# Kernel optimization log

Hardware: AMD Instinct MI355X
Metric: run time of the kernel (lower is better)

The kernel has to match this reference:

```python
import jax, jax.numpy as jnp
import numpy as np

N_NODES = 20000
N_EDGES = 320000
D_IN = 256
D_HID = 256
D_OUT = 128
N_LAYERS = 5
BN_EPS = 1e-5
W_SCALE = 1.0 / np.sqrt(D_HID)


def setup_inputs() -> dict:
    key = jax.random.key(0)
    ks = jax.random.split(key, 16)
    x = jax.random.normal(ks[0], (N_NODES, D_IN), dtype=jnp.float32)
    edge_index = jax.random.randint(ks[1], (2, N_EDGES), 0, N_NODES, dtype=jnp.int32)
    W1 = jax.random.normal(ks[2], (N_LAYERS, D_IN, D_HID), dtype=jnp.float32) * W_SCALE
    b1 = jax.random.normal(ks[3], (N_LAYERS, D_HID), dtype=jnp.float32) * 0.01
    W2a = jax.random.normal(ks[4], (N_LAYERS - 1, D_HID, D_HID), dtype=jnp.float32) * W_SCALE
    b2a = jax.random.normal(ks[5], (N_LAYERS - 1, D_HID), dtype=jnp.float32) * 0.01
    W2_last = jax.random.normal(ks[6], (D_HID, D_OUT), dtype=jnp.float32) * W_SCALE
    b2_last = jax.random.normal(ks[7], (D_OUT,), dtype=jnp.float32) * 0.01
    eps = jnp.zeros((N_LAYERS,), dtype=jnp.float32)
    bn_gamma = jnp.ones((N_LAYERS - 1, D_HID), dtype=jnp.float32)
    bn_beta = jnp.zeros((N_LAYERS - 1, D_HID), dtype=jnp.float32)
    bn_mean = jax.random.normal(ks[8], (N_LAYERS - 1, D_HID), dtype=jnp.float32) * 0.1
    bn_var = jax.random.uniform(ks[9], (N_LAYERS - 1, D_HID), dtype=jnp.float32, minval=0.5, maxval=1.5)
    return {"x": x, "edge_index": edge_index, "W1": W1, "b1": b1, "W2a": W2a,
            "b2a": b2a, "W2_last": W2_last, "b2_last": b2_last, "eps": eps,
            "bn_gamma": bn_gamma, "bn_beta": bn_beta, "bn_mean": bn_mean, "bn_var": bn_var}


def reference(x, edge_index, W1, b1, W2a, b2a, W2_last, b2_last, eps,
              bn_gamma, bn_beta, bn_mean, bn_var):
    src, dst = edge_index[0], edge_index[1]
    n = x.shape[0]

    def gin_conv(h, e, w1, bb1, w2, bb2):
        # scatter-add neighbor sum: agg[v] = sum_{(u->v)} h[u]
        agg = jax.ops.segment_sum(h[src], dst, num_segments=n)  # [N, d]
        z = (1.0 + e) * h + agg
        z = jax.nn.relu(z @ w1 + bb1)
        return z @ w2 + bb2

    h = x
    for i in range(N_LAYERS - 1):
        h = gin_conv(h, eps[i], W1[i], b1[i], W2a[i], b2a[i])
        # BatchNorm1d in eval mode (running stats); dropout inactive at inference
        h = (h - bn_mean[i]) * jax.lax.rsqrt(bn_var[i] + BN_EPS) * bn_gamma[i] + bn_beta[i]
        h = jax.nn.relu(h)
    out = gin_conv(h, eps[N_LAYERS - 1], W1[N_LAYERS - 1], b1[N_LAYERS - 1], W2_last, b2_last)
    return out
```

## Files before the change

kernel.cpp:

```cpp
#include <hip/hip_runtime.h>
#include <stdint.h>

#define NN    20000
#define NE    320000
#define MPAD  20096
#define DD    256
#define DOUT  128
#define CAP   64
#define RS    40
#define SS    1288
#define STS   264
#define SFS   132

typedef unsigned short u16;
typedef __attribute__((ext_vector_type(8))) __bf16 bf16x8;
typedef __attribute__((ext_vector_type(4))) float  f32x4;

__device__ __forceinline__ uint32_t f2b(float f){
  union { float f; uint32_t u; } x; x.f = f;
  uint32_t r = x.u + 0x7FFFu + ((x.u >> 16) & 1u);
  return r >> 16;
}
__device__ __forceinline__ float blo(uint32_t p){ union{uint32_t u;float f;}x; x.u=p<<16;         return x.f; }
__device__ __forceinline__ float bhi(uint32_t p){ union{uint32_t u;float f;}x; x.u=p&0xFFFF0000u; return x.f; }
__device__ __forceinline__ int   fiu(float f){ union{float f;int i;}x; x.f=f; return x.i; }
__device__ __forceinline__ float uif(int i){ union{int i;float f;}x; x.i=i; return x.f; }

#define TB 152
#define XB (MPAD/4)
#define EB ((NE+255)/256)
__global__ __launch_bounds__(256) void prep_all(
    const float* __restrict__ x, const int* __restrict__ src, const int* __restrict__ dst,
    const float* __restrict__ W1, const float* __restrict__ W2a, const float* __restrict__ W2l,
    u16* __restrict__ W1t, u16* __restrict__ W2at, u16* __restrict__ W2lt,
    u16* __restrict__ h0, int* __restrict__ cnt, int* __restrict__ csr)
{
  __shared__ u16 Ts[64][65];
  int b = blockIdx.x, tid = threadIdx.x;
  if (b < TB){
    const float* srcp; u16* dstp; int ldS, k0, n0;
    if (b < 80){
      int layer = b >> 4, sub = b & 15;
      srcp = W1 + layer*65536; dstp = W1t + layer*65536; ldS = 256;
      k0 = (sub >> 2)*64; n0 = (sub & 3)*64;
    } else if (b < 144){
      int bb = b - 80; int layer = bb >> 4, sub = bb & 15;
      srcp = W2a + layer*65536; dstp = W2at + layer*65536; ldS = 256;
      k0 = (sub >> 2)*64; n0 = (sub & 3)*64;
    } else {
      int sub = b - 144;
      srcp = W2l; dstp = W2lt; ldS = 128;
      k0 = (sub >> 1)*64; n0 = (sub & 1)*64;
    }
    int c = tid & 63, r0 = tid >> 6;
    #pragma unroll
    for (int i = 0; i < 16; ++i){
      int r = r0 + i*4;
      Ts[r][c] = (u16)f2b(srcp[(size_t)(k0 + r)*ldS + n0 + c]);
    }
    __syncthreads();
    #pragma unroll
    for (int i = 0; i < 16; ++i){
      int n = r0 + i*4;
      dstp[(size_t)(n0 + n)*256 + k0 + c] = Ts[c][n];
    }
  } else if (b < TB + XB){
    int bb = b - TB;
    int row  = bb*4 + (tid >> 6);
    int lane = tid & 63;
    uint2 o = make_uint2(0u, 0u);
    if (row < NN){
      float4 f = *(const float4*)(x + (size_t)row*DD + lane*4);
      o.x = f2b(f.x) | (f2b(f.y) << 16);
      o.y = f2b(f.z) | (f2b(f.w) << 16);
    }
    *(uint2*)(h0 + (size_t)row*DD + lane*4) = o;
  } else {
    int e = (b - TB - XB)*256 + tid;
    if (e < NE){
      int d = dst[e];
      int slot = atomicAdd(&cnt[d], 1);
      if (slot < CAP) csr[d*CAP + slot] = src[e];
    }
  }
}

__global__ __launch_bounds__(256, 3) void gin_fused(
    const u16* __restrict__ hin, const int* __restrict__ cnt, const int* __restrict__ csr,
    const float* __restrict__ eps_arr, int layer,
    const u16* __restrict__ w1, const float* __restrict__ b1,
    const u16* __restrict__ w2, const float* __restrict__ b2,
    const float* __restrict__ gma, const float* __restrict__ bta,
    const float* __restrict__ mu,  const float* __restrict__ var,
    u16* __restrict__ hout, float* __restrict__ outf, int last)
{
  __shared__ __align__(16) u16 As[8*SS];
  int tid  = threadIdx.x;
  int lane = tid & 63, w = tid >> 6;
  int m0 = blockIdx.x * 32;
  int l15 = lane & 15, l4 = lane >> 4;

  {
    float e = 1.0f + eps_arr[layer];
    int half = lane >> 5, kl = lane & 31;
    int xi = (lane ^ 32) << 2;
    const u16* hrow = hin + kl*8;
    u16* dstL = As + (kl >> 2)*SS + (kl & 3)*8;
    for (int i = 0; i < 8; ++i){
      int row = w*8 + i;
      int v = __builtin_amdgcn_readfirstlane(m0 + row);
      float a0=0.f,a1=0.f,a2=0.f,a3=0.f,a4=0.f,a5=0.f,a6=0.f,a7=0.f;
      if (v < NN){
        uint4 ov = *(const uint4*)(hrow + (size_t)v*DD);
        int deg = cnt[v]; deg = deg > CAP ? CAP : deg;
        const int* lst = csr + (size_t)v*CAP;
        for (int base = 0; base < deg; base += 16){
          int4 q[4];
          #pragma unroll
          for (int c = 0; c < 4; ++c) q[c] = *(const int4*)(lst + base + 4*c);
          int idv[8];
          #pragma unroll
          for (int c = 0; c < 4; ++c){
            idv[2*c]   = half ? q[c].y : q[c].x;
            idv[2*c+1] = half ? q[c].w : q[c].z;
          }
          uint4 rv[8];
          #pragma unroll
          for (int c = 0; c < 8; ++c){
            int g = (base + 2*c + half < deg) ? idv[c] : v;
            rv[c] = *(const uint4*)(hrow + (size_t)g*DD);
          }
          #pragma unroll
          for (int c = 0; c < 8; ++c){
            if (base + 2*c + half < deg){
              a0 += blo(rv[c].x); a1 += bhi(rv[c].x);
              a2 += blo(rv[c].y); a3 += bhi(rv[c].y);
              a4 += blo(rv[c].z); a5 += bhi(rv[c].z);
              a6 += blo(rv[c].w); a7 += bhi(rv[c].w);
            }
          }
        }
        float eh = half ? 0.0f : e;
        a0 += eh*blo(ov.x); a1 += eh*bhi(ov.x);
        a2 += eh*blo(ov.y); a3 += eh*bhi(ov.y);
        a4 += eh*blo(ov.z); a5 += eh*bhi(ov.z);
        a6 += eh*blo(ov.w); a7 += eh*bhi(ov.w);
      }
      a0 += uif(__builtin_amdgcn_ds_bpermute(xi, fiu(a0)));
      a1 += uif(__builtin_amdgcn_ds_bpermute(xi, fiu(a1)));
      a2 += uif(__builtin_amdgcn_ds_bpermute(xi, fiu(a2)));
      a3 += uif(__builtin_amdgcn_ds_bpermute(xi, fiu(a3)));
      a4 += uif(__builtin_amdgcn_ds_bpermute(xi, fiu(a4)));
      a5 += uif(__builtin_amdgcn_ds_bpermute(xi, fiu(a5)));
      a6 += uif(__builtin_amdgcn_ds_bpermute(xi, fiu(a6)));
      a7 += uif(__builtin_amdgcn_ds_bpermute(xi, fiu(a7)));
      if (half == 0){
        uint4 o;
        o.x = f2b(a0) | (f2b(a1) << 16);
        o.y = f2b(a2) | (f2b(a3) << 16);
        o.z = f2b(a4) | (f2b(a5) << 16);
        o.w = f2b(a6) | (f2b(a7) << 16);
        *(uint4*)(dstL + row*RS) = o;
      }
    }
  }
  __syncthreads();

  f32x4 acc1[4][2];
  #pragma unroll
  for (int i=0;i<4;++i)
    #pragma unroll
    for (int j=0;j<2;++j){ f32x4 zr={0.f,0.f,0.f,0.f}; acc1[i][j]=zr; }
  {
    int hidb = w*64;
    for (int s = 0; s < 8; ++s){
      bf16x8 af[4], bz[2];
      #pragma unroll
      for (int mi=0;mi<4;++mi)
        af[mi] = *(const bf16x8*)(w1 + (size_t)(hidb + mi*16 + l15)*DD + s*32 + l4*8);
      #pragma unroll
      for (int nj=0;nj<2;++nj)
        bz[nj] = *(const bf16x8*)(As + s*SS + (nj*16 + l15)*RS + l4*8);
      #pragma unroll
      for (int mi=0;mi<4;++mi)
        #pragma unroll
        for (int nj=0;nj<2;++nj)
          acc1[mi][nj] = __builtin_amdgcn_mfma_f32_16x16x32_bf16(af[mi], bz[nj], acc1[mi][nj], 0,0,0);
    }
  }
  __syncthreads();

  {
    int hidb = w*64;
    #pragma unroll
    for (int mi=0;mi<4;++mi){
      float4 bv = *(const float4*)(b1 + hidb + mi*16 + l4*4);
      int s2 = w*2 + (mi >> 1);
      int kp = (mi & 1)*16 + l4*4;
      #pragma unroll
      for (int nj=0;nj<2;++nj){
        int zrow = nj*16 + l15;
        float v0 = acc1[mi][nj][0] + bv.x; v0 = v0 > 0.f ? v0 : 0.f;
        float v1 = acc1[mi][nj][1] + bv.y; v1 = v1 > 0.f ? v1 : 0.f;
        float v2 = acc1[mi][nj][2] + bv.z; v2 = v2 > 0.f ? v2 : 0.f;
        float v3 = acc1[mi][nj][3] + bv.w; v3 = v3 > 0.f ? v3 : 0.f;
        uint2 pk;
        pk.x = f2b(v0) | (f2b(v1) << 16);
        pk.y = f2b(v2) | (f2b(v3) << 16);
        *(uint2*)(As + s2*SS + zrow*RS + kp) = pk;
      }
    }
  }
  __syncthreads();

  if (!last){
    f32x4 acc2[2][4];
    #pragma unroll
    for (int i=0;i<2;++i)
      #pragma unroll
      for (int j=0;j<4;++j){ f32x4 zr={0.f,0.f,0.f,0.f}; acc2[i][j]=zr; }
    int cb = w*64;
    for (int s = 0; s < 8; ++s){
      bf16x8 at[2], bw[4];
      #pragma unroll
      for (int i=0;i<2;++i)
        at[i] = *(const bf16x8*)(As + s*SS + (i*16 + l15)*RS + l4*8);
      #pragma unroll
      for (int j=0;j<4;++j)
        bw[j] = *(const bf16x8*)(w2 + (size_t)(cb + j*16 + l15)*DD + s*32 + l4*8);
      #pragma unroll
      for (int i=0;i<2;++i)
        #pragma unroll
        for (int j=0;j<4;++j)
          acc2[i][j] = __builtin_amdgcn_mfma_f32_16x16x32_bf16(at[i], bw[j], acc2[i][j], 0,0,0);
    }
    __syncthreads();
    u16* St = As;
    #pragma unroll
    for (int j=0;j<4;++j){
      int col = cb + j*16 + l15;
      float sc = rsqrtf(var[col] + 1e-5f) * gma[col];
      float sh = (b2[col] - mu[col]) * sc + bta[col];
      #pragma unroll
      for (int i=0;i<2;++i){
        #pragma unroll
        for (int r=0;r<4;++r){
          int row = i*16 + l4*4 + r;
          float vv = acc2[i][j][r]*sc + sh;
          vv = vv > 0.f ? vv : 0.f;
          St[row*STS + col] = (u16)f2b(vv);
        }
      }
    }
    __syncthreads();
    #pragma unroll
    for (int it = 0; it < 4; ++it){
      int idx = it*256 + tid;
      int row = idx >> 5, c = idx & 31;
      *(uint4*)(hout + (size_t)(m0 + row)*DD + c*8) = *(const uint4*)(St + row*STS + c*8);
    }
  } else {
    f32x4 acc2[2][2];
    #pragma unroll
    for (int i=0;i<2;++i)
      #pragma unroll
      for (int j=0;j<2;++j){ f32x4 zr={0.f,0.f,0.f,0.f}; acc2[i][j]=zr; }
    int cbk = w*32;
    for (int s = 0; s < 8; ++s){
      bf16x8 at[2], bw[2];
      #pragma unroll
      for (int i=0;i<2;++i)
        at[i] = *(const bf16x8*)(As + s*SS + (i*16 + l15)*RS + l4*8);
      #pragma unroll
      for (int j=0;j<2;++j)
        bw[j] = *(const bf16x8*)(w2 + (size_t)(cbk + j*16 + l15)*DD + s*32 + l4*8);
      #pragma unroll
      for (int i=0;i<2;++i)
        #pragma unroll
        for (int j=0;j<2;++j)
          acc2[i][j] = __builtin_amdgcn_mfma_f32_16x16x32_bf16(at[i], bw[j], acc2[i][j], 0,0,0);
    }
    __syncthreads();
    float* Sf = (float*)As;
    #pragma unroll
    for (int j=0;j<2;++j){
      int col = cbk + j*16 + l15;
      float sh = b2[col];
      #pragma unroll
      for (int i=0;i<2;++i){
        #pragma unroll
        for (int r=0;r<4;++r){
          int row = i*16 + l4*4 + r;
          Sf[row*SFS + col] = acc2[i][j][r] + sh;
        }
      }
    }
    __syncthreads();
    #pragma unroll
    for (int it = 0; it < 4; ++it){
      int idx = it*256 + tid;
      int row = idx >> 5, c = idx & 31;
      if (m0 + row < NN)
        *(uint4*)(outf + (size_t)(m0 + row)*DOUT + c*4) = *(const uint4*)(Sf + row*SFS + c*4);
    }
  }
}

extern "C" void kernel_launch(void* const* d_in, const int* in_sizes, int n_in,
                              void* d_out, int out_size, void* d_ws, size_t ws_size,
                              hipStream_t stream)
{
  const float* x     = (const float*)d_in[0];
  const int*   ei    = (const int*)  d_in[1];
  const float* W1    = (const float*)d_in[2];
  const float* b1    = (const float*)d_in[3];
  const float* W2a   = (const float*)d_in[4];
  const float* b2a   = (const float*)d_in[5];
  const float* W2l   = (const float*)d_in[6];
  const float* b2l   = (const float*)d_in[7];
  const float* eps   = (const float*)d_in[8];
  const float* gma   = (const float*)d_in[9];
  const float* bta   = (const float*)d_in[10];
  const float* mu    = (const float*)d_in[11];
  const float* var   = (const float*)d_in[12];
  float* out = (float*)d_out;

  char* ws = (char*)d_ws;
  size_t off = 0;
  auto alloc = [&](size_t bytes)->void*{
    void* p = ws + off; off += (bytes + 255) & ~(size_t)255; return p;
  };
  u16* h0   = (u16*)alloc((size_t)MPAD*DD*2);
  u16* h1   = (u16*)alloc((size_t)MPAD*DD*2);
  int* cnt  = (int*)alloc((size_t)NN*4);
  int* csr  = (int*)alloc((size_t)NN*CAP*4 + 64);
  u16* W1t  = (u16*)alloc((size_t)5*65536*2);
  u16* W2at = (u16*)alloc((size_t)4*65536*2);
  u16* W2lt = (u16*)alloc((size_t)32768*2);

  const int* srcA = ei;
  const int* dstA = ei + NE;

  hipMemsetAsync(cnt, 0, (size_t)NN*4, stream);
  prep_all<<<TB + XB + EB, 256, 0, stream>>>(x, srcA, dstA, W1, W2a, W2l,
                                             W1t, W2at, W2lt, h0, cnt, csr);

  u16* hbuf[2] = { h0, h1 };
  for (int L = 0; L < 5; ++L){
    const u16* hin = hbuf[L & 1];
    u16*       ho  = hbuf[1 - (L & 1)];
    if (L < 4){
      gin_fused<<<MPAD/32, 256, 0, stream>>>(hin, cnt, csr, eps, L,
          W1t + (size_t)L*65536, b1 + L*256,
          W2at + (size_t)L*65536, b2a + L*256,
          gma + L*256, bta + L*256, mu + L*256, var + L*256,
          ho, nullptr, 0);
    } else {
      gin_fused<<<MPAD/32, 256, 0, stream>>>(hin, cnt, csr, eps, L,
          W1t + (size_t)L*65536, b1 + L*256,
          W2lt, b2l,
          nullptr, nullptr, nullptr, nullptr,
          nullptr, out, 1);
    }
  }
}
```

Baseline: 330.0 us.

## Use 512-thread blocks and prefetch neighbor lists for all rows upfront

Doubles the block to 8 waves so each wave aggregates 4 rows instead of 8 and owns half as many output columns in both GEMMs. The first 16 CSR entries and the degree of each of the wave's 4 rows are loaded before any gathering starts, which exposes more memory-level parallelism. cnt/csr are padded to MPAD so that padded rows can be read without bounds checks. The cost is higher register pressure under launch_bounds(512,4) and that padded rows now read their own zero-degree lists.

```diff
diff --git a/kernel.cpp b/kernel.cpp
--- a/kernel.cpp
+++ b/kernel.cpp
@@ -85,7 +85,7 @@
   }
 }
 
-__global__ __launch_bounds__(256, 3) void gin_fused(
+__global__ __launch_bounds__(512, 4) void gin_fused(
     const u16* __restrict__ hin, const int* __restrict__ cnt, const int* __restrict__ csr,
     const float* __restrict__ eps_arr, int layer,
     const u16* __restrict__ w1, const float* __restrict__ b1,
@@ -106,46 +106,79 @@
     int xi = (lane ^ 32) << 2;
     const u16* hrow = hin + kl*8;
     u16* dstL = As + (kl >> 2)*SS + (kl & 3)*8;
-    for (int i = 0; i < 8; ++i){
-      int row = w*8 + i;
-      int v = __builtin_amdgcn_readfirstlane(m0 + row);
+    int vb = m0 + w*4;
+    int deg[4];
+    int4 q[4][4];
+    #pragma unroll
+    for (int n = 0; n < 4; ++n){
+      int v = vb + n;
+      int d = cnt[v];
+      deg[n] = d > CAP ? CAP : d;
+      const int4* lq = (const int4*)(csr + (size_t)v*CAP);
+      #pragma unroll
+      for (int c = 0; c < 4; ++c) q[n][c] = lq[c];
+    }
+    #pragma unroll
+    for (int n = 0; n < 4; ++n){
+      int v = vb + n;
+      int row = w*4 + n;
       float a0=0.f,a1=0.f,a2=0.f,a3=0.f,a4=0.f,a5=0.f,a6=0.f,a7=0.f;
-      if (v < NN){
-        uint4 ov = *(const uint4*)(hrow + (size_t)v*DD);
-        int deg = cnt[v]; deg = deg > CAP ? CAP : deg;
-        const int* lst = csr + (size_t)v*CAP;
-        for (int base = 0; base < deg; base += 16){
-          int4 q[4];
-          #pragma unroll
-          for (int c = 0; c < 4; ++c) q[c] = *(const int4*)(lst + base + 4*c);
-          int idv[8];
-          #pragma unroll
-          for (int c = 0; c < 4; ++c){
-            idv[2*c]   = half ? q[c].y : q[c].x;
-            idv[2*c+1] = half ? q[c].w : q[c].z;
+      uint4 ov = *(const uint4*)(hrow + (size_t)v*DD);
+      {
+        int idv[8];
+        #pragma unroll
+        for (int c = 0; c < 4; ++c){
+          idv[2*c]   = half ? q[n][c].y : q[n][c].x;
+          idv[2*c+1] = half ? q[n][c].w : q[n][c].z;
+        }
+        uint4 rv[8];
+        #pragma unroll
+        for (int c = 0; c < 8; ++c){
+          int g = (2*c + half < deg[n]) ? idv[c] : v;
+          rv[c] = *(const uint4*)(hrow + (size_t)g*DD);
+        }
+        #pragma unroll
+        for (int c = 0; c < 8; ++c){
+          if (2*c + half < deg[n]){
+            a0 += blo(rv[c].x); a1 += bhi(rv[c].x);
+            a2 += blo(rv[c].y); a3 += bhi(rv[c].y);
+            a4 += blo(rv[c].z); a5 += bhi(rv[c].z);
+            a6 += blo(rv[c].w); a7 += bhi(rv[c].w);
           }
-          uint4 rv[8];
-          #pragma unroll
-          for (int c = 0; c < 8; ++c){
-            int g = (base + 2*c + half < deg) ? idv[c] : v;
-            rv[c] = *(const uint4*)(hrow + (size_t)g*DD);
+        }
+      }
+      const int4* lq = (const int4*)(csr + (size_t)v*CAP);
+      for (int base = 16; base < deg[n]; base += 16){
+        int4 p[4];
+        #pragma unroll
+        for (int c = 0; c < 4; ++c) p[c] = lq[(base >> 2) + c];
+        int idv[8];
+        #pragma unroll
+        for (int c = 0; c < 4; ++c){
+          idv[2*c]   = half ? p[c].y : p[c].x;
+          idv[2*c+1] = half ? p[c].w : p[c].z;
+        }
+        uint4 rv[8];
+        #pragma unroll
+        for (int c = 0; c < 8; ++c){
+          int g = (base + 2*c + half < deg[n]) ? idv[c] : v;
+          rv[c] = *(const uint4*)(hrow + (size_t)g*DD);
+        }
+        #pragma unroll
+        for (int c = 0; c < 8; ++c){
+          if (base + 2*c + half < deg[n]){
+            a0 += blo(rv[c].x); a1 += bhi(rv[c].x);
+            a2 += blo(rv[c].y); a3 += bhi(rv[c].y);
+            a4 += blo(rv[c].z); a5 += bhi(rv[c].z);
+            a6 += blo(rv[c].w); a7 += bhi(rv[c].w);
           }
-          #pragma unroll
-          for (int c = 0; c < 8; ++c){
-            if (base + 2*c + half < deg){
-              a0 += blo(rv[c].x); a1 += bhi(rv[c].x);
-              a2 += blo(rv[c].y); a3 += bhi(rv[c].y);
-              a4 += blo(rv[c].z); a5 += bhi(rv[c].z);
-              a6 += blo(rv[c].w); a7 += bhi(rv[c].w);
-            }
-          }
-        }
-        float eh = half ? 0.0f : e;
-        a0 += eh*blo(ov.x); a1 += eh*bhi(ov.x);
-        a2 += eh*blo(ov.y); a3 += eh*bhi(ov.y);
-        a4 += eh*blo(ov.z); a5 += eh*bhi(ov.z);
-        a6 += eh*blo(ov.w); a7 += eh*bhi(ov.w);
-      }
+        }
+      }
+      float eh = (half == 0 && v < NN) ? e : 0.0f;
+      a0 += eh*blo(ov.x); a1 += eh*bhi(ov.x);
+      a2 += eh*blo(ov.y); a3 += eh*bhi(ov.y);
+      a4 += eh*blo(ov.z); a5 += eh*bhi(ov.z);
+      a6 += eh*blo(ov.w); a7 += eh*bhi(ov.w);
       a0 += uif(__builtin_amdgcn_ds_bpermute(xi, fiu(a0)));
       a1 += uif(__builtin_amdgcn_ds_bpermute(xi, fiu(a1)));
       a2 += uif(__builtin_amdgcn_ds_bpermute(xi, fiu(a2)));
@@ -166,23 +199,23 @@
   }
   __syncthreads();
 
-  f32x4 acc1[4][2];
+  f32x4 acc1[2][2];
   #pragma unroll
-  for (int i=0;i<4;++i)
+  for (int i=0;i<2;++i)
     #pragma unroll
     for (int j=0;j<2;++j){ f32x4 zr={0.f,0.f,0.f,0.f}; acc1[i][j]=zr; }
   {
-    int hidb = w*64;
+    int hidb = w*32;
     for (int s = 0; s < 8; ++s){
-      bf16x8 af[4], bz[2];
-      #pragma unroll
-      for (int mi=0;mi<4;++mi)
+      bf16x8 af[2], bz[2];
+      #pragma unroll
+      for (int mi=0;mi<2;++mi)
         af[mi] = *(const bf16x8*)(w1 + (size_t)(hidb + mi*16 + l15)*DD + s*32 + l4*8);
       #pragma unroll
       for (int nj=0;nj<2;++nj)
         bz[nj] = *(const bf16x8*)(As + s*SS + (nj*16 + l15)*RS + l4*8);
       #pragma unroll
-      for (int mi=0;mi<4;++mi)
+      for (int mi=0;mi<2;++mi)
         #pragma unroll
         for (int nj=0;nj<2;++nj)
           acc1[mi][nj] = __builtin_amdgcn_mfma_f32_16x16x32_bf16(af[mi], bz[nj], acc1[mi][nj], 0,0,0);
@@ -191,12 +224,11 @@
   __syncthreads();
 
   {
-    int hidb = w*64;
-    #pragma unroll
-    for (int mi=0;mi<4;++mi){
+    int hidb = w*32;
+    #pragma unroll
+    for (int mi=0;mi<2;++mi){
       float4 bv = *(const float4*)(b1 + hidb + mi*16 + l4*4);
-      int s2 = w*2 + (mi >> 1);
-      int kp = (mi & 1)*16 + l4*4;
+      int kp = mi*16 + l4*4;
       #pragma unroll
       for (int nj=0;nj<2;++nj){
         int zrow = nj*16 + l15;
@@ -207,37 +239,37 @@
         uint2 pk;
         pk.x = f2b(v0) | (f2b(v1) << 16);
         pk.y = f2b(v2) | (f2b(v3) << 16);
-        *(uint2*)(As + s2*SS + zrow*RS + kp) = pk;
+        *(uint2*)(As + w*SS + zrow*RS + kp) = pk;
       }
     }
   }
   __syncthreads();
 
   if (!last){
-    f32x4 acc2[2][4];
+    f32x4 acc2[2][2];
     #pragma unroll
     for (int i=0;i<2;++i)
       #pragma unroll
-      for (int j=0;j<4;++j){ f32x4 zr={0.f,0.f,0.f,0.f}; acc2[i][j]=zr; }
-    int cb = w*64;
+      for (int j=0;j<2;++j){ f32x4 zr={0.f,0.f,0.f,0.f}; acc2[i][j]=zr; }
+    int cb = w*32;
     for (int s = 0; s < 8; ++s){
-      bf16x8 at[2], bw[4];
+      bf16x8 at[2], bw[2];
       #pragma unroll
       for (int i=0;i<2;++i)
         at[i] = *(const bf16x8*)(As + s*SS + (i*16 + l15)*RS + l4*8);
       #pragma unroll
-      for (int j=0;j<4;++j)
+      for (int j=0;j<2;++j)
         bw[j] = *(const bf16x8*)(w2 + (size_t)(cb + j*16 + l15)*DD + s*32 + l4*8);
       #pragma unroll
       for (int i=0;i<2;++i)
         #pragma unroll
-        for (int j=0;j<4;++j)
+        for (int j=0;j<2;++j)
           acc2[i][j] = __builtin_amdgcn_mfma_f32_16x16x32_bf16(at[i], bw[j], acc2[i][j], 0,0,0);
     }
     __syncthreads();
     u16* St = As;
     #pragma unroll
-    for (int j=0;j<4;++j){
+    for (int j=0;j<2;++j){
       int col = cb + j*16 + l15;
       float sc = rsqrtf(var[col] + 1e-5f) * gma[col];
       float sh = (b2[col] - mu[col]) * sc + bta[col];
@@ -254,51 +286,44 @@
     }
     __syncthreads();
     #pragma unroll
-    for (int it = 0; it < 4; ++it){
-      int idx = it*256 + tid;
+    for (int it = 0; it < 2; ++it){
+      int idx = it*512 + tid;
       int row = idx >> 5, c = idx & 31;
       *(uint4*)(hout + (size_t)(m0 + row)*DD + c*8) = *(const uint4*)(St + row*STS + c*8);
     }
   } else {
-    f32x4 acc2[2][2];
-    #pragma unroll
-    for (int i=0;i<2;++i)
-      #pragma unroll
-      for (int j=0;j<2;++j){ f32x4 zr={0.f,0.f,0.f,0.f}; acc2[i][j]=zr; }
-    int cbk = w*32;
+    f32x4 acc2[2];
+    #pragma unroll
+    for (int i=0;i<2;++i){ f32x4 zr={0.f,0.f,0.f,0.f}; acc2[i]=zr; }
+    int cbk = w*16;
     for (int s = 0; s < 8; ++s){
-      bf16x8 at[2], bw[2];
+      bf16x8 at[2], bw;
       #pragma unroll
       for (int i=0;i<2;++i)
         at[i] = *(const bf16x8*)(As + s*SS + (i*16 + l15)*RS + l4*8);
-      #pragma unroll
-      for (int j=0;j<2;++j)
-        bw[j] = *(const bf16x8*)(w2 + (size_t)(cbk + j*16 + l15)*DD + s*32 + l4*8);
+      bw = *(const bf16x8*)(w2 + (size_t)(cbk + l15)*DD + s*32 + l4*8);
       #pragma unroll
       for (int i=0;i<2;++i)
-        #pragma unroll
-        for (int j=0;j<2;++j)
-          acc2[i][j] = __builtin_amdgcn_mfma_f32_16x16x32_bf16(at[i], bw[j], acc2[i][j], 0,0,0);
+        acc2[i] = __builtin_amdgcn_mfma_f32_16x16x32_bf16(at[i], bw, acc2[i], 0,0,0);
     }
     __syncthreads();
     float* Sf = (float*)As;
-    #pragma unroll
-    for (int j=0;j<2;++j){
-      int col = cbk + j*16 + l15;
+    {
+      int col = cbk + l15;
       float sh = b2[col];
       #pragma unroll
       for (int i=0;i<2;++i){
         #pragma unroll
         for (int r=0;r<4;++r){
           int row = i*16 + l4*4 + r;
-          Sf[row*SFS + col] = acc2[i][j][r] + sh;
-        }
-      }
-    }
-    __syncthreads();
-    #pragma unroll
-    for (int it = 0; it < 4; ++it){
-      int idx = it*256 + tid;
+          Sf[row*SFS + col] = acc2[i][r] + sh;
+        }
+      }
+    }
+    __syncthreads();
+    #pragma unroll
+    for (int it = 0; it < 2; ++it){
+      int idx = it*512 + tid;
       int row = idx >> 5, c = idx & 31;
       if (m0 + row < NN)
         *(uint4*)(outf + (size_t)(m0 + row)*DOUT + c*4) = *(const uint4*)(Sf + row*SFS + c*4);
@@ -332,8 +357,8 @@
   };
   u16* h0   = (u16*)alloc((size_t)MPAD*DD*2);
   u16* h1   = (u16*)alloc((size_t)MPAD*DD*2);
-  int* cnt  = (int*)alloc((size_t)NN*4);
-  int* csr  = (int*)alloc((size_t)NN*CAP*4 + 64);
+  int* cnt  = (int*)alloc((size_t)MPAD*4);
+  int* csr  = (int*)alloc((size_t)MPAD*CAP*4 + 64);
   u16* W1t  = (u16*)alloc((size_t)5*65536*2);
   u16* W2at = (u16*)alloc((size_t)4*65536*2);
   u16* W2lt = (u16*)alloc((size_t)32768*2);
@@ -341,7 +366,7 @@
   const int* srcA = ei;
   const int* dstA = ei + NE;
 
-  hipMemsetAsync(cnt, 0, (size_t)NN*4, stream);
+  hipMemsetAsync(cnt, 0, (size_t)MPAD*4, stream);
   prep_all<<<TB + XB + EB, 256, 0, stream>>>(x, srcA, dstA, W1, W2a, W2l,
                                              W1t, W2at, W2lt, h0, cnt, csr);
 
@@ -350,13 +375,13 @@
     const u16* hin = hbuf[L & 1];
     u16*       ho  = hbuf[1 - (L & 1)];
     if (L < 4){
-      gin_fused<<<MPAD/32, 256, 0, stream>>>(hin, cnt, csr, eps, L,
+      gin_fused<<<MPAD/32, 512, 0, stream>>>(hin, cnt, csr, eps, L,
           W1t + (size_t)L*65536, b1 + L*256,
           W2at + (size_t)L*65536, b2a + L*256,
           gma + L*256, bta + L*256, mu + L*256, var + L*256,
           ho, nullptr, 0);
     } else {
-      gin_fused<<<MPAD/32, 256, 0, stream>>>(hin, cnt, csr, eps, L,
+      gin_fused<<<MPAD/32, 512, 0, stream>>>(hin, cnt, csr, eps, L,
           W1t + (size_t)L*65536, b1 + L*256,
           W2lt, b2l,
           nullptr, nullptr, nullptr, nullptr,
```

Result: slower. 358.5 us (+8.6%).
